# Kernel optimization log

Measured on AMD Instinct MI355X. Metric: run time of the kernel, lower is better.

The kernel has to match this reference:

```python
import jax, jax.numpy as jnp
import numpy as np

B, H, C, D, HID = 32, 100, 50, 400, 400


def setup_inputs() -> dict:
    key = jax.random.key(0)
    k0, k1, k2, k3, k4, k5 = jax.random.split(key, 6)
    hist_news_vector = jax.random.normal(k0, (B, H, D), jnp.float32)
    cand_news_vector = jax.random.normal(k1, (B, C, D), jnp.float32)
    mask_hist = jax.random.bernoulli(k2, 0.9, (B, H))
    mask_cand = jax.random.bernoulli(k3, 0.9, (B, C))
    # dnn params: Linear(2D -> HID) then Linear(HID -> 1) (no activation in between, as in source)
    W1 = (jax.random.normal(k4, (2 * D, HID), jnp.float32) * 0.02)
    b1 = jnp.zeros((HID,), jnp.float32)
    w2 = (jax.random.normal(k5, (HID,), jnp.float32) * 0.02)
    b2 = jnp.zeros((), jnp.float32)
    return dict(hist_news_vector=hist_news_vector, cand_news_vector=cand_news_vector,
                mask_hist=mask_hist, mask_cand=mask_cand, W1=W1, b1=b1, w2=w2, b2=b2)


def reference(hist_news_vector, cand_news_vector, mask_hist, mask_cand, W1, b1, w2, b2):
    d = cand_news_vector.shape[-1]
    # concat order in source is [cand, hist]; split W1 so we never materialize the [B,C,H,2D] concat
    W1c, W1h = W1[:d], W1[d:]
    cand_part = cand_news_vector @ W1c            # [B, C, HID]
    hist_part = hist_news_vector @ W1h            # [B, H, HID]
    h = cand_part[:, :, None, :] + hist_part[:, None, :, :] + b1   # [B, C, H, HID]
    scores = h @ w2 + b2                          # [B, C, H]
    neg = jnp.finfo(scores.dtype).min
    scores = jnp.where(mask_hist[:, None, :], scores, neg)
    weights = jax.nn.softmax(scores, axis=-1)     # softmax over hist dim
    weights = jnp.where(mask_cand[:, :, None], weights, jnp.zeros((), weights.dtype))
    user_vector = jnp.einsum('bch,bhd->bcd', weights, hist_news_vector)  # [B, C, D]
    return user_vector
```

## Files before the change

kernel.cpp:

```cpp
#include <hip/hip_runtime.h>
#include <math.h>

#define B_   32
#define H_   100
#define C_   50
#define D_   400
#define HID_ 400

#define NEGF (-3.4028234663852886e38f)


__global__ __launch_bounds__(512)
void k1_u(const float* __restrict__ W1, const float* __restrict__ w2,
          float* __restrict__ u) {
    const int row  = blockIdx.x * 8 + (threadIdx.x >> 6);
    const int lane = threadIdx.x & 63;
    const float* wrow = W1 + (size_t)(D_ + row) * HID_;
    float acc = 0.f;
    #pragma unroll
    for (int j = lane; j < HID_; j += 64)
        acc = fmaf(wrow[j], w2[j], acc);
    #pragma unroll
    for (int off = 32; off; off >>= 1)
        acc += __shfl_xor(acc, off, 64);
    if (lane == 0) u[row] = acc;
}

__global__ __launch_bounds__(512)
void k2_s(const float* __restrict__ hist, const int* __restrict__ mask_hist,
          const float* __restrict__ u, float* __restrict__ s) {
    const int row  = blockIdx.x * 8 + (threadIdx.x >> 6);
    const int lane = threadIdx.x & 63;
    const float* hrow = hist + (size_t)row * D_;
    float acc = 0.f;
    #pragma unroll
    for (int j = lane; j < D_; j += 64)
        acc = fmaf(hrow[j], u[j], acc);
    #pragma unroll
    for (int off = 32; off; off >>= 1)
        acc += __shfl_xor(acc, off, 64);
    if (lane == 0) s[row] = mask_hist[row] ? acc : NEGF;
}

#define NTILES 7

__global__ __launch_bounds__(256)
void k3_out(const float* __restrict__ hist, const float* __restrict__ s,
            const int* __restrict__ mask_cand, float* __restrict__ out) {
    __shared__ float w_lds[128];
    __shared__ float part[4][64];
    __shared__ float uv_lds[64];

    const int b    = blockIdx.x / NTILES;
    const int tile = blockIdx.x % NTILES;
    const int d0   = tile * 64;
    const int lane = threadIdx.x & 63;
    const int wave = threadIdx.x >> 6;
    const int d    = d0 + lane;

    const float* sb = s + b * H_;
    const float s0 = sb[lane];
    const float s1 = (lane + 64 < H_) ? sb[lane + 64] : -INFINITY;
    float m = fmaxf(s0, s1);
    #pragma unroll
    for (int off = 32; off; off >>= 1)
        m = fmaxf(m, __shfl_xor(m, off, 64));
    const float e0 = expf(s0 - m);
    const float e1 = (lane + 64 < H_) ? expf(s1 - m) : 0.f;
    float ps = e0 + e1;
    #pragma unroll
    for (int off = 32; off; off >>= 1)
        ps += __shfl_xor(ps, off, 64);
    const float inv = 1.f / ps;

    if (wave == 0) {
        w_lds[lane] = e0 * inv;
        if (lane + 64 < H_) w_lds[lane + 64] = e1 * inv;
    }
    __syncthreads();

    const float* hb = hist + (size_t)b * H_ * D_;
    float acc = 0.f;
    if (d < D_) {
        const int h0 = wave * 25;
        #pragma unroll
        for (int i = 0; i < 25; i++)
            acc = fmaf(w_lds[h0 + i], hb[(h0 + i) * D_ + d], acc);
    }
    part[wave][lane] = acc;
    __syncthreads();
    if (wave == 0)
        uv_lds[lane] = part[0][lane] + part[1][lane] + part[2][lane] + part[3][lane];
    __syncthreads();

    const float uv = uv_lds[lane];
    const int* mcb = mask_cand + b * C_;
    float* outb = out + (size_t)b * C_ * D_ + d0;
    if (d < D_) {
        for (int c = wave; c < C_; c += 4)
            outb[(size_t)c * D_ + lane] = mcb[c] ? uv : 0.f;
    }
}

extern "C" void kernel_launch(void* const* d_in, const int* in_sizes, int n_in,
                              void* d_out, int out_size, void* d_ws, size_t ws_size,
                              hipStream_t stream) {
    const float* hist      = (const float*)d_in[0];
    const int*   mask_hist = (const int*)d_in[2];
    const int*   mask_cand = (const int*)d_in[3];
    const float* W1        = (const float*)d_in[4];
    const float* w2        = (const float*)d_in[6];
    float* out = (float*)d_out;

    float* u = (float*)d_ws;
    float* s = u + D_;

    k1_u  <<<D_ / 8,        512, 0, stream>>>(W1, w2, u);
    k2_s  <<<(B_ * H_) / 8, 512, 0, stream>>>(hist, mask_hist, u, s);
    k3_out<<<B_ * NTILES,   256, 0, stream>>>(hist, s, mask_cand, out);
}
```

Measured before the change: 17.05 us.

## Fuse hist scoring into softmax/output kernel and vectorize dot products

Merges the per-history score kernel into the softmax-weighted-sum kernel, so each block recomputes the scores for its batch into LDS. This drops one kernel launch and the global round trip for the scores. Row dot products now use float4 loads, and the block index is remapped to interleave batches. The cost is that each of the 7 tiles per batch recomputes all 100 scores, which adds redundant reads of hist.

Result: slower. 26.96 us (+58.1%).

```diff
diff --git a/kernel.cpp b/kernel.cpp
--- a/kernel.cpp
+++ b/kernel.cpp
@@ -6,6 +6,7 @@
 #define C_   50
 #define D_   400
 #define HID_ 400
+#define NTILES 7
 
 #define NEGF (-3.4028234663852886e38f)
 
@@ -15,90 +16,94 @@
           float* __restrict__ u) {
     const int row  = blockIdx.x * 8 + (threadIdx.x >> 6);
     const int lane = threadIdx.x & 63;
-    const float* wrow = W1 + (size_t)(D_ + row) * HID_;
-    float acc = 0.f;
+    const float4* r4 = (const float4*)(W1 + (size_t)(D_ + row) * HID_);
+    const float4* w4 = (const float4*)w2;
+    float4 a0 = r4[lane];
+    float4 b0 = w4[lane];
+    float acc = a0.x*b0.x + a0.y*b0.y + a0.z*b0.z + a0.w*b0.w;
+    if (lane < 36) {
+        float4 a1 = r4[64 + lane];
+        float4 b1 = w4[64 + lane];
+        acc += a1.x*b1.x + a1.y*b1.y + a1.z*b1.z + a1.w*b1.w;
+    }
     #pragma unroll
-    for (int j = lane; j < HID_; j += 64)
-        acc = fmaf(wrow[j], w2[j], acc);
-    #pragma unroll
-    for (int off = 32; off; off >>= 1)
-        acc += __shfl_xor(acc, off, 64);
+    for (int off = 32; off; off >>= 1) acc += __shfl_xor(acc, off, 64);
     if (lane == 0) u[row] = acc;
 }
 
-__global__ __launch_bounds__(512)
-void k2_s(const float* __restrict__ hist, const int* __restrict__ mask_hist,
-          const float* __restrict__ u, float* __restrict__ s) {
-    const int row  = blockIdx.x * 8 + (threadIdx.x >> 6);
-    const int lane = threadIdx.x & 63;
-    const float* hrow = hist + (size_t)row * D_;
-    float acc = 0.f;
-    #pragma unroll
-    for (int j = lane; j < D_; j += 64)
-        acc = fmaf(hrow[j], u[j], acc);
-    #pragma unroll
-    for (int off = 32; off; off >>= 1)
-        acc += __shfl_xor(acc, off, 64);
-    if (lane == 0) s[row] = mask_hist[row] ? acc : NEGF;
-}
+__global__ __launch_bounds__(256)
+void k2_fused(const float* __restrict__ hist, const float* __restrict__ u,
+              const int* __restrict__ mask_hist, const int* __restrict__ mask_cand,
+              float* __restrict__ out) {
+    __shared__ float s_lds[H_];
+    __shared__ float w_lds[H_];
+    __shared__ float part[4][64];
 
-#define NTILES 7
-
-__global__ __launch_bounds__(256)
-void k3_out(const float* __restrict__ hist, const float* __restrict__ s,
-            const int* __restrict__ mask_cand, float* __restrict__ out) {
-    __shared__ float w_lds[128];
-    __shared__ float part[4][64];
-    __shared__ float uv_lds[64];
-
-    const int b    = blockIdx.x / NTILES;
-    const int tile = blockIdx.x % NTILES;
+    const int x    = blockIdx.x & 7;
+    const int k    = blockIdx.x >> 3;
+    const int q    = k / 7;
+    const int b    = x + 8 * q;
+    const int tile = k - 7 * q;
     const int d0   = tile * 64;
     const int lane = threadIdx.x & 63;
     const int wave = threadIdx.x >> 6;
-    const int d    = d0 + lane;
 
-    const float* sb = s + b * H_;
-    const float s0 = sb[lane];
-    const float s1 = (lane + 64 < H_) ? sb[lane + 64] : -INFINITY;
-    float m = fmaxf(s0, s1);
-    #pragma unroll
-    for (int off = 32; off; off >>= 1)
-        m = fmaxf(m, __shfl_xor(m, off, 64));
-    const float e0 = expf(s0 - m);
-    const float e1 = (lane + 64 < H_) ? expf(s1 - m) : 0.f;
-    float ps = e0 + e1;
-    #pragma unroll
-    for (int off = 32; off; off >>= 1)
-        ps += __shfl_xor(ps, off, 64);
-    const float inv = 1.f / ps;
+    const float* hb = hist + (size_t)b * H_ * D_;
 
-    if (wave == 0) {
-        w_lds[lane] = e0 * inv;
-        if (lane + 64 < H_) w_lds[lane + 64] = e1 * inv;
+    const float4* u4 = (const float4*)u;
+    float4 ua = u4[lane];
+    float4 ub = (lane < 36) ? u4[64 + lane] : make_float4(0.f, 0.f, 0.f, 0.f);
+
+    const int* mh = mask_hist + b * H_;
+    for (int i = 0; i < 25; i++) {
+        const int h = wave * 25 + i;
+        const float4* r4 = (const float4*)(hb + (size_t)h * D_);
+        float4 a = r4[lane];
+        float acc = a.x*ua.x + a.y*ua.y + a.z*ua.z + a.w*ua.w;
+        if (lane < 36) {
+            float4 a1 = r4[64 + lane];
+            acc += a1.x*ub.x + a1.y*ub.y + a1.z*ub.z + a1.w*ub.w;
+        }
+        #pragma unroll
+        for (int off = 32; off; off >>= 1) acc += __shfl_xor(acc, off, 64);
+        if (lane == 0) s_lds[h] = mh[h] ? acc : NEGF;
     }
     __syncthreads();
 
-    const float* hb = hist + (size_t)b * H_ * D_;
+    const float s0 = s_lds[lane];
+    const float s1 = (lane < 36) ? s_lds[lane + 64] : -INFINITY;
+    float m = fmaxf(s0, s1);
+    #pragma unroll
+    for (int off = 32; off; off >>= 1) m = fmaxf(m, __shfl_xor(m, off, 64));
+    const float e0 = expf(s0 - m);
+    const float e1 = (lane < 36) ? expf(s1 - m) : 0.f;
+    float ps = e0 + e1;
+    #pragma unroll
+    for (int off = 32; off; off >>= 1) ps += __shfl_xor(ps, off, 64);
+    const float inv = 1.f / ps;
+    if (wave == 0) {
+        w_lds[lane] = e0 * inv;
+        if (lane < 36) w_lds[lane + 64] = e1 * inv;
+    }
+    __syncthreads();
+
+    const int d = d0 + lane;
     float acc = 0.f;
     if (d < D_) {
         const int h0 = wave * 25;
         #pragma unroll
         for (int i = 0; i < 25; i++)
-            acc = fmaf(w_lds[h0 + i], hb[(h0 + i) * D_ + d], acc);
+            acc = fmaf(w_lds[h0 + i], hb[(size_t)(h0 + i) * D_ + d], acc);
     }
     part[wave][lane] = acc;
     __syncthreads();
-    if (wave == 0)
-        uv_lds[lane] = part[0][lane] + part[1][lane] + part[2][lane] + part[3][lane];
-    __syncthreads();
 
-    const float uv = uv_lds[lane];
-    const int* mcb = mask_cand + b * C_;
+    const float uv = part[0][lane] + part[1][lane] + part[2][lane] + part[3][lane];
+    const int* mc  = mask_cand + b * C_;
     float* outb = out + (size_t)b * C_ * D_ + d0;
     if (d < D_) {
         for (int c = wave; c < C_; c += 4)
-            outb[(size_t)c * D_ + lane] = mcb[c] ? uv : 0.f;
+            outb[(size_t)c * D_ + lane] = mc[c] ? uv : 0.f;
     }
 }
 
@@ -113,9 +118,7 @@
     float* out = (float*)d_out;
 
     float* u = (float*)d_ws;
-    float* s = u + D_;
 
-    k1_u  <<<D_ / 8,        512, 0, stream>>>(W1, w2, u);
-    k2_s  <<<(B_ * H_) / 8, 512, 0, stream>>>(hist, mask_hist, u, s);
-    k3_out<<<B_ * NTILES,   256, 0, stream>>>(hist, s, mask_cand, out);
+    k1_u    <<<D_ / 8,      512, 0, stream>>>(W1, w2, u);
+    k2_fused<<<B_ * NTILES, 256, 0, stream>>>(hist, u, mask_hist, mask_cand, out);
 }
```
